# Kernel optimization log

Measured on AMD Instinct MI355X. Metric: run time of the kernel, lower is better.

Reference implementation:

```python
import jax, jax.numpy as jnp
import numpy as np

# Dims
B, C, D, H, W = 2, 64, 16, 64, 64
G = 2            # deformable groups (choose_group(64, 2) -> 2)
K = 27           # 3x3x3 kernel points
GC = C // G      # channels per group
AXIS = (0.5, 1.0, 1.0)   # offset_axis_scale (d, h, w)
EPS = 1e-5
# kernel point offsets for k=3, pad=1, dilation=1: {-1,0,1}^3
_KOFF = np.array([(a, b, c) for a in (-1, 0, 1) for b in (-1, 0, 1) for c in (-1, 0, 1)], dtype=np.float32)


def conv3d(x, w, b=None, pad=0):
    y = jax.lax.conv_general_dilated(x, w, (1, 1, 1), [(pad, pad)] * 3,
                                     dimension_numbers=('NCDHW', 'OIDHW', 'NCDHW'))
    if b is not None:
        y = y + b[None, :, None, None, None]
    return y


def proj1x1(x, w, b=None):
    y = jnp.einsum('oc,bcdhw->bodhw', w, x)
    if b is not None:
        y = y + b[None, :, None, None, None]
    return y


def _trilinear_sample(vflat, pd, ph, pw):
    # vflat: [B,G,GC,DHW]; pd/ph/pw: [B,G,DHW] float sampling coords; zeros padding outside
    d0 = jnp.floor(pd); h0 = jnp.floor(ph); w0 = jnp.floor(pw)
    td, th, tw = pd - d0, ph - h0, pw - w0
    d0 = d0.astype(jnp.int32); h0 = h0.astype(jnp.int32); w0 = w0.astype(jnp.int32)
    acc = jnp.zeros_like(vflat)
    for dd in (0, 1):
        for hh in (0, 1):
            for ww in (0, 1):
                di, hi, wi = d0 + dd, h0 + hh, w0 + ww
                valid = ((di >= 0) & (di < D) & (hi >= 0) & (hi < H) & (wi >= 0) & (wi < W)).astype(vflat.dtype)
                idx = (jnp.clip(di, 0, D - 1) * H + jnp.clip(hi, 0, H - 1)) * W + jnp.clip(wi, 0, W - 1)
                g = jnp.take_along_axis(vflat, jnp.broadcast_to(idx[:, :, None, :], vflat.shape), axis=3)
                wgt = ((td if dd else 1.0 - td) * (th if hh else 1.0 - th) * (tw if ww else 1.0 - tw)) * valid
                acc = acc + g * wgt[:, :, None, :]
    return acc


def setup_inputs() -> dict:
    key = jax.random.key(0)
    ks = jax.random.split(key, 8)
    f = jnp.float32
    s = 1.0 / np.sqrt(C)
    return {
        'x': jax.random.normal(ks[0], (B, C, D, H, W), f),
        'gate': jnp.zeros((), f),
        'pre_w': jax.random.normal(ks[1], (C, C, 1, 1, 1), f) * s,
        'post_w': jax.random.normal(ks[2], (C, C, 1, 1, 1), f) * s,
        'in_proj_w': jax.random.normal(ks[3], (C, C), f) * s,
        'in_proj_b': jnp.zeros((C,), f),
        'out_proj_w': jax.random.normal(ks[4], (C, C), f) * s,
        'out_proj_b': jnp.zeros((C,), f),
        'off_w': jax.random.normal(ks[5], (3 * G * K, C, 3, 3, 3), f) * 0.01,
        'off_b': jnp.zeros((3 * G * K,), f),
        'mask_w': jax.random.normal(ks[6], (G * K, C, 3, 3, 3), f) * 0.01,
        'mask_b': jnp.zeros((G * K,), f),
        'in_gamma': jnp.ones((C,), f),
        'in_beta': jnp.zeros((C,), f),
    }


def reference(x, gate, pre_w, post_w, in_proj_w, in_proj_b, out_proj_w, out_proj_b,
              off_w, off_b, mask_w, mask_b, in_gamma, in_beta):
    DHW = D * H * W
    xp = conv3d(x, pre_w)                                      # pre 1x1
    # --- DCNv3_3D: value projection, learned offsets + softmax modulation mask ---
    v = proj1x1(xp, in_proj_w, in_proj_b).reshape(B, G, GC, DHW)
    off = conv3d(xp, off_w, off_b, pad=1).reshape(B, G, K, 3, DHW)   # warmed-up offset_scale = 1.0
    m = jax.nn.softmax(conv3d(xp, mask_w, mask_b, pad=1).reshape(B, G, K, DHW), axis=2)
    dg, hg, wg = jnp.meshgrid(jnp.arange(D, dtype=jnp.float32),
                              jnp.arange(H, dtype=jnp.float32),
                              jnp.arange(W, dtype=jnp.float32), indexing='ij')
    dg, hg, wg = dg.reshape(-1), hg.reshape(-1), wg.reshape(-1)      # [DHW]
    out = jnp.zeros_like(v)
    for k in range(K):   # fixed small loop over 27 kernel points
        pd = dg + _KOFF[k, 0] + off[:, :, k, 0] * AXIS[0]
        ph = hg + _KOFF[k, 1] + off[:, :, k, 1] * AXIS[1]
        pw = wg + _KOFF[k, 2] + off[:, :, k, 2] * AXIS[2]
        out = out + _trilinear_sample(v, pd, ph, pw) * m[:, :, k, :][:, :, None, :]
    y = out.reshape(B, C, D, H, W)
    y = proj1x1(y, out_proj_w, out_proj_b)
    # InstanceNorm3d + GELU
    mu = y.mean(axis=(2, 3, 4), keepdims=True)
    var = y.var(axis=(2, 3, 4), keepdims=True)
    y = (y - mu) * jax.lax.rsqrt(var + EPS)
    y = y * in_gamma[None, :, None, None, None] + in_beta[None, :, None, None, None]
    y = jax.nn.gelu(y)
    y = conv3d(y, post_w)                                      # post 1x1
    return x + jax.nn.sigmoid(gate) * y
```

## Files before the change

kernel.cpp:

```cpp
#include <hip/hip_runtime.h>
#include <hip/hip_bf16.h>

typedef short short8 __attribute__((ext_vector_type(8)));
typedef float f32x4 __attribute__((ext_vector_type(4)));
typedef _Float16 h2 __attribute__((ext_vector_type(2)));
typedef __fp16 fp16x2 __attribute__((ext_vector_type(2)));

#if __has_builtin(__builtin_elementwise_fma)
#define FMA2H(a, b, c) __builtin_elementwise_fma((a), (b), (c))
#else
#define FMA2H(a, b, c) ((a) * (b) + (c))
#endif

namespace {
constexpr int Bn = 2, Cn = 64, Dn = 16, Hn = 64, Wn = 64;
constexpr int Gn = 2, Kn = 27, GCn = 32;
constexpr int DHW = Dn * Hn * Wn;
constexpr int OCn = 216;
constexpr int PD = 18, PH = 66, PW = 66;
constexpr float EPS = 1e-5f;

constexpr int SROWS = 4 * 66;
constexpr int SLICE_B = SROWS * 128;

constexpr size_t XPADH_OFF = 0;
constexpr size_t XPADH_B   = (size_t)Bn * PD * PH * PW * Cn * 2;
constexpr size_t WFRAG_OFF = XPADH_OFF + XPADH_B;
constexpr size_t WFRAG_B   = (size_t)54 * 16 * 64 * 16;
constexpr size_t WV_OFF    = WFRAG_OFF + WFRAG_B;
constexpr size_t WV_B      = 64 * 64 * 4;
constexpr size_t CONV_OFF  = WV_OFF + WV_B;
constexpr size_t CONV_B    = (size_t)Bn * OCn * DHW * 2;
constexpr size_t V_OFF     = CONV_OFF + CONV_B;
constexpr size_t V_B       = (size_t)Bn * Gn * DHW * GCn * 2;
constexpr size_t SAMP_OFF  = V_OFF + V_B;
constexpr size_t SAMP_B    = (size_t)Bn * Gn * DHW * GCn * 2;
constexpr size_t STAT_OFF  = SAMP_OFF + SAMP_B;
constexpr size_t VBH_OFF   = STAT_OFF + 4096;
constexpr size_t VFRAG_OFF = VBH_OFF + 256;
constexpr size_t OFRAG_OFF = VFRAG_OFF + 8192;
constexpr size_t PFRAG_OFF = OFRAG_OFF + 8192;
}

__device__ inline float b2f(short s) {
  union { float f; unsigned u; } x; x.u = ((unsigned)(unsigned short)s) << 16; return x.f;
}
__device__ inline short f2b(float f) {
  __hip_bfloat16 h = __float2bfloat16(f);
  union { __hip_bfloat16 h; short s; } x; x.h = h; return x.s;
}
__device__ inline int iclamp(int v, int lo, int hi) { return v < lo ? lo : (v > hi ? hi : v); }
__device__ inline h2 u2h2(unsigned u) {
  union { unsigned u; h2 h; } x; x.u = u; return x.h;
}
__device__ inline unsigned h2u(h2 h) {
  union { unsigned u; h2 h; } x; x.h = h; return x.u;
}
__device__ inline h2 pkrtz(float a, float b) {
#if __has_builtin(__builtin_amdgcn_cvt_pkrtz)
  union { fp16x2 p; h2 h; } x;
  x.p = __builtin_amdgcn_cvt_pkrtz(a, b);
  return x.h;
#else
  return (h2){(_Float16)a, (_Float16)b};
#endif
}

__global__ __launch_bounds__(256) void zerofill(uint4* __restrict__ p, int n16) {
  int i = blockIdx.x * 256 + threadIdx.x;
  if (i < n16) p[i] = make_uint4(0, 0, 0, 0);
}

__global__ __launch_bounds__(256) void fillpad(const float* __restrict__ x,
                                               __hip_bfloat16* __restrict__ xpadh) {
  int tid = threadIdx.x;
  int w5 = tid & 31, cq = tid >> 5;
  int p = blockIdx.x * 32 + w5;
  int b = blockIdx.y;
  int w = p & 63, h = (p >> 6) & 63, d = p >> 12;
  const float* xb = x + ((size_t)b * 64 + cq * 8) * DHW + p;
  short8 o8;
#pragma unroll
  for (int j = 0; j < 8; ++j) o8[j] = f2b(xb[(size_t)j * DHW]);
  __hip_bfloat16* ob = xpadh + (size_t)b * (PD * PH * PW * 64)
      + ((((size_t)(d + 1) * 66) + (h + 1)) * 66 + (w + 1)) * 64 + cq * 8;
  *(short8*)ob = o8;
}

__global__ __launch_bounds__(256) void fold_weights(
    const float* __restrict__ pre_w, const float* __restrict__ in_proj_w,
    const float* __restrict__ off_w, const float* __restrict__ mask_w,
    short8* __restrict__ Wfrag, float* __restrict__ Wv) {
  int i = blockIdx.x * 256 + threadIdx.x;
  if (i < 64 * 64) {
    int o = i >> 6, c = i & 63;
    float s = 0.f;
    for (int cp = 0; cp < 64; ++cp) s += in_proj_w[o * 64 + cp] * pre_w[cp * 64 + c];
    Wv[i] = s;
    return;
  }
  int t = i - 64 * 64;
  if (t >= 54 * 16 * 64) return;
  int l = t & 63; int rest = t >> 6;
  int mt = rest & 15; int ks = rest >> 4;
  int oc = mt * 16 + (l & 15);
  int tap = ks >> 1;
  int c0 = (ks & 1) * 32 + (l >> 4) * 8;
  float vals[8] = {0.f, 0.f, 0.f, 0.f, 0.f, 0.f, 0.f, 0.f};
  if (oc < OCn) {
    const float* cw = (oc < 162) ? (off_w + (size_t)oc * 64 * 27)
                                 : (mask_w + (size_t)(oc - 162) * 64 * 27);
#pragma unroll 1
    for (int cp = 0; cp < 64; ++cp) {
      float wv = cw[cp * 27 + tap];
      const float* pr = pre_w + cp * 64 + c0;
#pragma unroll
      for (int j = 0; j < 8; ++j) vals[j] += wv * pr[j];
    }
  }
  short8 o8;
#pragma unroll
  for (int j = 0; j < 8; ++j) o8[j] = f2b(vals[j]);
  Wfrag[t] = o8;
}

__global__ __launch_bounds__(256) void packfrag(
    const float* __restrict__ Wv, const float* __restrict__ Wout,
    const float* __restrict__ Wpost, const float* __restrict__ vb,
    short8* __restrict__ vfrag, short8* __restrict__ ofrag,
    short8* __restrict__ pfrag, h2* __restrict__ vbh) {
  int i = blockIdx.x * 256 + threadIdx.x;
  if (i < 32) vbh[i] = pkrtz(vb[2 * i], vb[2 * i + 1]);
  int which = i >> 9;
  int t = i & 511;
  int l = t & 63, mt = (t >> 6) & 3, ks = t >> 8;
  int m = mt * 16 + (l & 15);
  int k0 = ks * 32 + (l >> 4) * 8;
  const float* W = (which == 0) ? Wv : (which == 1) ? Wout : Wpost;
  short8 o;
#pragma unroll
  for (int j = 0; j < 8; ++j) o[j] = f2b(W[m * 64 + k0 + j]);
  if (which == 0) vfrag[t] = o;
  else if (which == 1) ofrag[t] = o;
  else pfrag[t] = o;
}

#define GEMM_MFMA_BODY(FRAG)                                                  \
  int wid = tid >> 6, l = tid & 63, lm = l & 15, lk = l >> 4;                 \
  f32x4 acc[4][4];                                                            \
  _Pragma("unroll")                                                           \
  for (int mt = 0; mt < 4; ++mt)                                              \
    _Pragma("unroll")                                                         \
    for (int nt = 0; nt < 4; ++nt) acc[mt][nt] = (f32x4){0.f, 0.f, 0.f, 0.f}; \
  _Pragma("unroll")                                                           \
  for (int ks = 0; ks < 2; ++ks) {                                            \
    short8 af[4], bf[4];                                                      \
    _Pragma("unroll")                                                         \
    for (int mt = 0; mt < 4; ++mt) af[mt] = FRAG[(ks * 4 + mt) * 64 + l];     \
    _Pragma("unroll")                                                         \
    for (int nt = 0; nt < 4; ++nt) {                                          \
      int sr = wid * 64 + nt * 16 + lm;                                       \
      int us = ks * 4 + lk;                                                   \
      bf[nt] = *(const short8*)(stg + sr * 128 + ((us ^ (sr & 7)) << 4));     \
    }                                                                         \
    _Pragma("unroll")                                                         \
    for (int mt = 0; mt < 4; ++mt)                                            \
      _Pragma("unroll")                                                       \
      for (int nt = 0; nt < 4; ++nt)                                          \
        acc[mt][nt] = __builtin_amdgcn_mfma_f32_16x16x32_bf16(af[mt], bf[nt], acc[mt][nt], 0, 0, 0); \
  }

__global__ __launch_bounds__(256) void vproj_mfma(
    const char* __restrict__ xpadh, const short8* __restrict__ vfrag,
    const h2* __restrict__ vbh, _Float16* __restrict__ v) {
  __shared__ char stg[32768];
  __shared__ char bnc[256 * 144];
  int tid = threadIdx.x;
  int p0 = blockIdx.x * 256, b = blockIdx.y;
  const char* xb = xpadh + (size_t)b * (PD * PH * PW * 128);
#pragma unroll
  for (int it = 0; it < 8; ++it) {
    int idx = it * 256 + tid;
    int s = idx >> 3, slot = idx & 7;
    int p = p0 + s, w = p & 63, h = (p >> 6) & 63, d = p >> 12;
    const char* g = xb + ((((size_t)(d + 1)) * 66 + (h + 1)) * 66 + (w + 1)) * 128 + slot * 16;
    *(uint4*)(stg + s * 128 + ((slot ^ (s & 7)) << 4)) = *(const uint4*)g;
  }
  __syncthreads();
  GEMM_MFMA_BODY(vfrag)
#pragma unroll
  for (int mt = 0; mt < 4; ++mt)
#pragma unroll
    for (int nt = 0; nt < 4; ++nt)
#pragma unroll
      for (int r = 0; r < 4; ++r) {
        int pos = wid * 64 + nt * 16 + lm;
        int oc = mt * 16 + lk * 4 + r;
        *(_Float16*)(bnc + pos * 144 + oc * 2) = (_Float16)acc[mt][nt][r];
      }
  __syncthreads();
  {
    int p = p0 + tid;
    const unsigned* brow = (const unsigned*)(bnc + tid * 144);
    char* vb0 = (char*)v + ((size_t)(b * 2 + 0) * DHW + p) * 64;
    char* vb1 = (char*)v + ((size_t)(b * 2 + 1) * DHW + p) * 64;
#pragma unroll
    for (int s = 0; s < 8; ++s) {
      uint4 ov;
      unsigned* po = (unsigned*)&ov;
#pragma unroll
      for (int j = 0; j < 4; ++j) {
        h2 hv = u2h2(brow[s * 4 + j]) + vbh[s * 4 + j];
        po[j] = h2u(hv);
      }
      if (s < 4) *(uint4*)(vb0 + s * 16) = ov;
      else       *(uint4*)(vb1 + (s - 4) * 16) = ov;
    }
  }
}

__global__ __launch_bounds__(512, 4) void conv_mfma(
    const char* __restrict__ xpadh, const char* __restrict__ wfrag,
    const float* __restrict__ off_b, const float* __restrict__ mask_b,
    __hip_bfloat16* __restrict__ convout) {
  __shared__ char lds[SLICE_B];
  int tid = threadIdx.x;
  int h0 = blockIdx.x * 2, d = blockIdx.y, b = blockIdx.z;

  int wid = tid >> 6, l = tid & 63;
  int wm = wid & 3, wn = wid >> 2;
  int lm = l & 15, lk = l >> 4;
  const char* abase = wfrag + ((size_t)((wm * 4) * 64 + l)) * 16;
  const char* xb = xpadh + (size_t)b * (PD * PH * PW * 128);

  f32x4 acc[4][4];
#pragma unroll
  for (int mt = 0; mt < 4; ++mt)
#pragma unroll
    for (int nt = 0; nt < 4; ++nt) acc[mt][nt] = (f32x4){0.f, 0.f, 0.f, 0.f};

  short8 A0[4], B0[4];

#define LOADA(KS)                                                             \
  {                                                                           \
    const char* ap_ = abase + (KS) * 16384;                                   \
    _Pragma("unroll")                                                         \
    for (int mt = 0; mt < 4; ++mt) A0[mt] = *(const short8*)(ap_ + mt * 1024); \
  }
  LOADA(0)

#pragma unroll 1
  for (int dd = 0; dd < 3; ++dd) {
    __syncthreads();
#pragma unroll
    for (int it = 0; it < 5; ++it) {
      int idx = it * 512 + tid;
      if (idx < SROWS * 8) {
        int s = idx >> 3, slot = idx & 7;
        int hp = s / 66, wx = s - hp * 66;
        const char* g = xb + ((((size_t)(d + dd)) * 66 + (h0 + hp)) * 66 + wx) * 128 + slot * 16;
        *(uint4*)(lds + s * 128 + ((slot ^ (s & 7)) << 4)) = *(const uint4*)g;
      }
    }
    __syncthreads();

#pragma unroll 1
    for (int tl = 0; tl < 9; ++tl) {
      int dh = tl / 3, dw = tl - dh * 3;
      int srow = (wn + dh) * 66 + dw;
#pragma unroll
      for (int ch = 0; ch < 2; ++ch) {
        int ks = dd * 18 + tl * 2 + ch;
        int uslot = 4 * ch + lk;
#pragma unroll
        for (int nt = 0; nt < 4; ++nt) {
          int sr = srow + nt * 16 + lm;
          B0[nt] = *(const short8*)(lds + sr * 128 + ((uslot ^ (sr & 7)) << 4));
        }
        __builtin_amdgcn_s_setprio(1);
#pragma unroll
        for (int mt = 0; mt < 4; ++mt)
#pragma unroll
          for (int nt = 0; nt < 4; ++nt)
            acc[mt][nt] = __builtin_amdgcn_mfma_f32_16x16x32_bf16(A0[mt], B0[nt], acc[mt][nt], 0, 0, 0);
        __builtin_amdgcn_s_setprio(0);
        if (ks + 1 < 54) LOADA(ks + 1)
      }
    }
  }
#undef LOADA

  int pbase = d * 4096 + (h0 + wn) * 64;
#pragma unroll
  for (int mt = 0; mt < 4; ++mt) {
    int oc0 = wm * 64 + mt * 16 + lk * 4;
#pragma unroll
    for (int r = 0; r < 4; ++r) {
      int oc = oc0 + r;
      if (oc < OCn) {
        float bias = (oc < 162) ? off_b[oc] : mask_b[oc - 162];
        size_t orow = ((size_t)b * OCn + oc) * DHW + pbase;
#pragma unroll
        for (int nt = 0; nt < 4; ++nt)
          convout[orow + nt * 16 + lm] = __float2bfloat16(acc[mt][nt][r] + bias);
      }
    }
  }
}

__global__ __launch_bounds__(256) void dcn_sample(
    const __hip_bfloat16* __restrict__ convout, const _Float16* __restrict__ v,
    short* __restrict__ sampled) {
  __shared__ short offm[108 * 64];
  int tid = threadIdx.x;
  int id = blockIdx.x;
  int bg = (id & 7) >> 1;
  int p0 = (((id >> 3) << 1) + (id & 1)) * 64;
  int b = bg >> 1, g = bg & 1;

  const __hip_bfloat16* cb = convout + (size_t)b * OCn * DHW;
#pragma unroll 1
  for (int idx = tid; idx < 108 * 8; idx += 256) {
    int row = idx >> 3, col = idx & 7;
    int oc = (row < 81) ? (g * 81 + row) : (162 + g * Kn + (row - 81));
    *(uint4*)(offm + row * 64 + col * 8) = *(const uint4*)(cb + (size_t)oc * DHW + p0 + col * 8);
  }
  __syncthreads();

  int pl = tid >> 2, q = tid & 3;
  int p = p0 + pl;
  int w = p & 63, h = (p >> 6) & 63, d = p >> 12;

  float msum = 0.f;
  h2 acc[4];
#pragma unroll
  for (int j = 0; j < 4; ++j) acc[j] = (h2){(_Float16)0.f, (_Float16)0.f};
  const char* vg = (const char*)v + ((size_t)bg * DHW * GCn + q * 8) * 2;

#pragma unroll 1
  for (int k = 0; k < Kn; ++k) {
    float offd = b2f(offm[(3 * k + 0) * 64 + pl]);
    float offh = b2f(offm[(3 * k + 1) * 64 + pl]);
    float offw = b2f(offm[(3 * k + 2) * 64 + pl]);
    float pd = (float)(d + (k / 9) - 1) + offd * 0.5f;
    float ph = (float)(h + ((k / 3) % 3) - 1) + offh;
    float pw = (float)(w + (k % 3) - 1) + offw;
    float fd = floorf(pd), fh = floorf(ph), fw = floorf(pw);
    float td = pd - fd, th = ph - fh, tw = pw - fw;
    int d0 = (int)fd, h0 = (int)fh, w0 = (int)fw;
    float ek = __expf(b2f(offm[(81 + k) * 64 + pl]));
    msum += ek;

    float wd0 = ((unsigned)d0 < (unsigned)Dn) ? (1.f - td) * ek : 0.f;
    float wd1 = ((unsigned)(d0 + 1) < (unsigned)Dn) ? td * ek : 0.f;
    float wh0 = ((unsigned)h0 < (unsigned)Hn) ? (1.f - th) : 0.f;
    float wh1 = ((unsigned)(h0 + 1) < (unsigned)Hn) ? th : 0.f;
    float ww0 = ((unsigned)w0 < (unsigned)Wn) ? (1.f - tw) : 0.f;
    float ww1 = ((unsigned)(w0 + 1) < (unsigned)Wn) ? tw : 0.f;
    int dr0 = iclamp(d0, 0, Dn - 1) << 18, dr1 = iclamp(d0 + 1, 0, Dn - 1) << 18;
    int hr0 = iclamp(h0, 0, Hn - 1) << 12, hr1 = iclamp(h0 + 1, 0, Hn - 1) << 12;
    int wc0 = iclamp(w0, 0, Wn - 1) << 6,  wc1 = iclamp(w0 + 1, 0, Wn - 1) << 6;
    float wdh00 = wd0 * wh0, wdh01 = wd0 * wh1, wdh10 = wd1 * wh0, wdh11 = wd1 * wh1;

#define CORNER(BOFF, WT)                                                \
    {                                                                   \
      _Float16 wh_ = (_Float16)(WT);                                    \
      h2 w2_ = {wh_, wh_};                                              \
      uint4 u_ = *(const uint4*)(vg + (BOFF));                          \
      acc[0] = FMA2H(u2h2(u_.x), w2_, acc[0]);                          \
      acc[1] = FMA2H(u2h2(u_.y), w2_, acc[1]);                          \
      acc[2] = FMA2H(u2h2(u_.z), w2_, acc[2]);                          \
      acc[3] = FMA2H(u2h2(u_.w), w2_, acc[3]);                          \
    }
    CORNER(dr0 + hr0 + wc0, wdh00 * ww0)
    CORNER(dr0 + hr0 + wc1, wdh00 * ww1)
    CORNER(dr0 + hr1 + wc0, wdh01 * ww0)
    CORNER(dr0 + hr1 + wc1, wdh01 * ww1)
    CORNER(dr1 + hr0 + wc0, wdh10 * ww0)
    CORNER(dr1 + hr0 + wc1, wdh10 * ww1)
    CORNER(dr1 + hr1 + wc0, wdh11 * ww0)
    CORNER(dr1 + hr1 + wc1, wdh11 * ww1)
#undef CORNER
  }

  float rs = 1.f / msum;
  short8 o8;
#pragma unroll
  for (int j = 0; j < 4; ++j) {
    o8[2 * j]     = f2b((float)acc[j][0] * rs);
    o8[2 * j + 1] = f2b((float)acc[j][1] * rs);
  }
  *(short8*)((char*)sampled + ((size_t)bg * DHW + p) * 64 + q * 16) = o8;
}

__global__ __launch_bounds__(256) void outproj_mfma(
    const short* __restrict__ sampled, const short8* __restrict__ ofrag,
    const float* __restrict__ ob, __hip_bfloat16* __restrict__ t) {
  __shared__ char stg[32768];
  __shared__ char bnc[256 * 144];
  int tid = threadIdx.x;
  int p0 = blockIdx.x * 256, b = blockIdx.y;
#pragma unroll
  for (int it = 0; it < 8; ++it) {
    int idx = it * 256 + tid;
    int s = idx >> 3, slot = idx & 7;
    int g = slot >> 2;
    const char* src = (const char*)sampled + ((size_t)(b * 2 + g) * DHW + p0 + s) * 64 + (slot & 3) * 16;
    *(uint4*)(stg + s * 128 + ((slot ^ (s & 7)) << 4)) = *(const uint4*)src;
  }
  __syncthreads();
  GEMM_MFMA_BODY(ofrag)
#pragma unroll
  for (int mt = 0; mt < 4; ++mt)
#pragma unroll
    for (int r = 0; r < 4; ++r) {
      int oc = mt * 16 + lk * 4 + r;
      float bias = ob[oc];
#pragma unroll
      for (int nt = 0; nt < 4; ++nt) {
        int pos = wid * 64 + nt * 16 + lm;
        *(short*)(bnc + pos * 144 + oc * 2) = f2b(acc[mt][nt][r] + bias);
      }
    }
  __syncthreads();
  {
    int c = tid & 63, pq = tid >> 6;
    short* trow = (short*)t + ((size_t)b * 64 + c) * DHW + p0 + pq * 64;
#pragma unroll
    for (int s8 = 0; s8 < 8; ++s8) {
      short8 o8;
#pragma unroll
      for (int j = 0; j < 8; ++j)
        o8[j] = *(const short*)(bnc + (pq * 64 + s8 * 8 + j) * 144 + c * 2);
      *(short8*)(trow + s8 * 8) = o8;
    }
  }
}

__global__ __launch_bounds__(256) void stats_k(const __hip_bfloat16* __restrict__ t,
                                               float* __restrict__ stat) {
  int bc = blockIdx.x;
  const short8* tc = (const short8*)(t + (size_t)bc * DHW);
  float s = 0.f, ss = 0.f;
  for (int i = threadIdx.x; i < DHW / 8; i += 256) {
    short8 s8 = tc[i];
#pragma unroll
    for (int j = 0; j < 8; ++j) { float xv = b2f(s8[j]); s += xv; ss += xv * xv; }
  }
#pragma unroll
  for (int o = 32; o > 0; o >>= 1) { s += __shfl_down(s, o); ss += __shfl_down(ss, o); }
  __shared__ float ls[4], lss[4];
  int wid = threadIdx.x >> 6;
  if ((threadIdx.x & 63) == 0) { ls[wid] = s; lss[wid] = ss; }
  __syncthreads();
  if (threadIdx.x == 0) {
    float S = ls[0] + ls[1] + ls[2] + ls[3];
    float SS = lss[0] + lss[1] + lss[2] + lss[3];
    float mu = S / (float)DHW;
    float var = SS / (float)DHW - mu * mu;
    stat[bc * 2 + 0] = mu;
    stat[bc * 2 + 1] = rsqrtf(var + EPS);
  }
}

__global__ __launch_bounds__(256) void normgelu(
    const __hip_bfloat16* __restrict__ t, const float* __restrict__ stat,
    const float* __restrict__ gamma, const float* __restrict__ beta,
    short* __restrict__ nvh) {
  int p = blockIdx.x * 256 + threadIdx.x;
  int b = blockIdx.y;
  short o[64];
#pragma unroll
  for (int c = 0; c < Cn; ++c) {
    float mu = stat[(b * Cn + c) * 2 + 0];
    float rstd = stat[(b * Cn + c) * 2 + 1];
    float tv = b2f(((const short*)t)[((size_t)b * Cn + c) * DHW + p]);
    float yv = (tv - mu) * rstd * gamma[c] + beta[c];
    float u = 0.7978845608028654f * (yv + 0.044715f * yv * yv * yv);
    float e = __expf(2.f * u);
    float th = 1.f - 2.f / (e + 1.f);
    o[c] = f2b(0.5f * yv * (1.f + th));
  }
  short* dst = nvh + ((size_t)b * DHW + p) * 64;
#pragma unroll
  for (int s8 = 0; s8 < 8; ++s8) {
    short8 o8;
#pragma unroll
    for (int j = 0; j < 8; ++j) o8[j] = o[s8 * 8 + j];
    *(short8*)(dst + s8 * 8) = o8;
  }
}

__global__ __launch_bounds__(256) void post_mfma(
    const short* __restrict__ nvh, const short8* __restrict__ pfrag,
    const float* __restrict__ x, const float* __restrict__ gate,
    float* __restrict__ out) {
  __shared__ char stg[32768];
  __shared__ char bnc[256 * 144];
  int tid = threadIdx.x;
  int p0 = blockIdx.x * 256, b = blockIdx.y;
#pragma unroll
  for (int it = 0; it < 8; ++it) {
    int idx = it * 256 + tid;
    int s = idx >> 3, slot = idx & 7;
    const char* src = (const char*)nvh + ((size_t)b * DHW + p0 + s) * 128 + slot * 16;
    *(uint4*)(stg + s * 128 + ((slot ^ (s & 7)) << 4)) = *(const uint4*)src;
  }
  __syncthreads();
  GEMM_MFMA_BODY(pfrag)
#pragma unroll
  for (int mt = 0; mt < 4; ++mt)
#pragma unroll
    for (int nt = 0; nt < 4; ++nt)
#pragma unroll
      for (int r = 0; r < 4; ++r) {
        int pos = wid * 64 + nt * 16 + lm;
        int oc = mt * 16 + lk * 4 + r;
        *(short*)(bnc + pos * 144 + oc * 2) = f2b(acc[mt][nt][r]);
      }
  __syncthreads();
  {
    float sg = 1.f / (1.f + __expf(-gate[0]));
    int c = tid & 63, pq = tid >> 6;
    size_t base = ((size_t)b * 64 + c) * DHW + p0 + pq * 64;
    const float4* x4 = (const float4*)(x + base);
    float4* o4 = (float4*)(out + base);
#pragma unroll
    for (int qd = 0; qd < 16; ++qd) {
      float4 xv = x4[qd];
      float v0 = b2f(*(const short*)(bnc + (pq * 64 + qd * 4 + 0) * 144 + c * 2));
      float v1 = b2f(*(const short*)(bnc + (pq * 64 + qd * 4 + 1) * 144 + c * 2));
      float v2 = b2f(*(const short*)(bnc + (pq * 64 + qd * 4 + 2) * 144 + c * 2));
      float v3 = b2f(*(const short*)(bnc + (pq * 64 + qd * 4 + 3) * 144 + c * 2));
      o4[qd] = make_float4(xv.x + sg * v0, xv.y + sg * v1, xv.z + sg * v2, xv.w + sg * v3);
    }
  }
}

extern "C" void kernel_launch(void* const* d_in, const int* in_sizes, int n_in,
                              void* d_out, int out_size, void* d_ws, size_t ws_size,
                              hipStream_t stream) {
  const float* x          = (const float*)d_in[0];
  const float* gate       = (const float*)d_in[1];
  const float* pre_w      = (const float*)d_in[2];
  const float* post_w     = (const float*)d_in[3];
  const float* in_proj_w  = (const float*)d_in[4];
  const float* in_proj_b  = (const float*)d_in[5];
  const float* out_proj_w = (const float*)d_in[6];
  const float* out_proj_b = (const float*)d_in[7];
  const float* off_w      = (const float*)d_in[8];
  const float* off_b      = (const float*)d_in[9];
  const float* mask_w     = (const float*)d_in[10];
  const float* mask_b     = (const float*)d_in[11];
  const float* in_gamma   = (const float*)d_in[12];
  const float* in_beta    = (const float*)d_in[13];

  char* ws = (char*)d_ws;
  __hip_bfloat16* xpadh = (__hip_bfloat16*)(ws + XPADH_OFF);
  short8* Wfrag  = (short8*)(ws + WFRAG_OFF);
  float* Wv      = (float*)(ws + WV_OFF);
  __hip_bfloat16* convout = (__hip_bfloat16*)(ws + CONV_OFF);
  _Float16* v    = (_Float16*)(ws + V_OFF);
  short* sampled = (short*)(ws + SAMP_OFF);
  short* nvh     = (short*)(ws + SAMP_OFF);
  float* stat    = (float*)(ws + STAT_OFF);
  h2* vbh        = (h2*)(ws + VBH_OFF);
  short8* vfrag  = (short8*)(ws + VFRAG_OFF);
  short8* ofrag  = (short8*)(ws + OFRAG_OFF);
  short8* pfrag  = (short8*)(ws + PFRAG_OFF);
  __hip_bfloat16* t = (__hip_bfloat16*)(ws + XPADH_OFF);
  float* out = (float*)d_out;

  int zf16 = (int)(XPADH_B / 16);
  zerofill<<<(zf16 + 255) / 256, 256, 0, stream>>>((uint4*)xpadh, zf16);
  fillpad<<<dim3(DHW / 32, Bn), 256, 0, stream>>>(x, xpadh);
  int foldN = (64 * 64 + 54 * 16 * 64 + 255) / 256;
  fold_weights<<<foldN, 256, 0, stream>>>(pre_w, in_proj_w, off_w, mask_w, Wfrag, Wv);
  packfrag<<<6, 256, 0, stream>>>(Wv, out_proj_w, post_w, in_proj_b,
                                  vfrag, ofrag, pfrag, vbh);
  vproj_mfma<<<dim3(DHW / 256, Bn), 256, 0, stream>>>((const char*)xpadh, vfrag, vbh, v);
  conv_mfma<<<dim3(32, 16, 2), 512, 0, stream>>>((const char*)xpadh, (const char*)Wfrag,
                                                 off_b, mask_b, convout);
  dcn_sample<<<4096, 256, 0, stream>>>(convout, v, sampled);
  outproj_mfma<<<dim3(DHW / 256, Bn), 256, 0, stream>>>(sampled, ofrag, out_proj_b, t);
  stats_k<<<Bn * Cn, 256, 0, stream>>>(t, stat);
  normgelu<<<dim3(DHW / 256, Bn), 256, 0, stream>>>(t, stat, in_gamma, in_beta, nvh);
  post_mfma<<<dim3(DHW / 256, Bn), 256, 0, stream>>>(nvh, pfrag, x, gate, out);
}
```

Baseline: 328.1 us.

## Double-buffer conv LDS via global_load_lds and fuse norm stats into outproj

The conv kernel now double-buffers its input slice in LDS and fills it with direct global-to-LDS loads, so the next depth slice is fetched while the MFMAs for the current one run. This removes the load-then-sync stall at the start of each depth step. Separately, the per-channel sum and sum-of-squares for the instance norm are accumulated inside outproj via LDS and global atomics, which removes the stats_k kernel and its extra pass over t. The costs are double the LDS per conv block, which may lower occupancy, atomic contention on 256 stat entries, and float sums whose order is no longer deterministic.

```diff
diff --git a/kernel.cpp b/kernel.cpp
--- a/kernel.cpp
+++ b/kernel.cpp
@@ -11,6 +11,10 @@
 #else
 #define FMA2H(a, b, c) ((a) * (b) + (c))
 #endif
+
+typedef const unsigned int __attribute__((address_space(1))) u32_g;
+typedef unsigned int __attribute__((address_space(3))) u32_s;
+#define GLDS16(gp, lp) __builtin_amdgcn_global_load_lds((u32_g*)(gp), (u32_s*)(lp), 16, 0, 0)
 
 namespace {
 constexpr int Bn = 2, Cn = 64, Dn = 16, Hn = 64, Wn = 64;
@@ -128,9 +132,10 @@
     const float* __restrict__ Wv, const float* __restrict__ Wout,
     const float* __restrict__ Wpost, const float* __restrict__ vb,
     short8* __restrict__ vfrag, short8* __restrict__ ofrag,
-    short8* __restrict__ pfrag, h2* __restrict__ vbh) {
+    short8* __restrict__ pfrag, h2* __restrict__ vbh, float* __restrict__ stat) {
   int i = blockIdx.x * 256 + threadIdx.x;
   if (i < 32) vbh[i] = pkrtz(vb[2 * i], vb[2 * i + 1]);
+  if (i >= 256 && i < 512) stat[i - 256] = 0.f;
   int which = i >> 9;
   int t = i & 511;
   int l = t & 63, mt = (t >> 6) & 3, ks = t >> 8;
@@ -223,7 +228,7 @@
     const char* __restrict__ xpadh, const char* __restrict__ wfrag,
     const float* __restrict__ off_b, const float* __restrict__ mask_b,
     __hip_bfloat16* __restrict__ convout) {
-  __shared__ char lds[SLICE_B];
+  __shared__ char lds[2 * SLICE_B];
   int tid = threadIdx.x;
   int h0 = blockIdx.x * 2, d = blockIdx.y, b = blockIdx.z;
 
@@ -247,22 +252,31 @@
     _Pragma("unroll")                                                         \
     for (int mt = 0; mt < 4; ++mt) A0[mt] = *(const short8*)(ap_ + mt * 1024); \
   }
+#define STAGE(DD, BUF)                                                        \
+  {                                                                           \
+    char* db_ = lds + (BUF) * SLICE_B + (wid << 10);                          \
+    _Pragma("unroll")                                                         \
+    for (int it = 0; it < 5; ++it) {                                          \
+      int idx = it * 512 + tid;                                               \
+      if (idx < SROWS * 8) {                                                  \
+        int s_ = idx >> 3, slot_ = idx & 7;                                   \
+        int hp_ = s_ / 66, wx_ = s_ - hp_ * 66;                               \
+        int sslot_ = slot_ ^ (s_ & 7);                                        \
+        const char* g_ = xb + ((((size_t)(d + (DD))) * 66 + (h0 + hp_)) * 66 + wx_) * 128 + sslot_ * 16; \
+        GLDS16(g_, db_ + it * 8192);                                          \
+      }                                                                       \
+    }                                                                         \
+  }
+
+  STAGE(0, 0)
   LOADA(0)
+  __syncthreads();
 
 #pragma unroll 1
   for (int dd = 0; dd < 3; ++dd) {
-    __syncthreads();
-#pragma unroll
-    for (int it = 0; it < 5; ++it) {
-      int idx = it * 512 + tid;
-      if (idx < SROWS * 8) {
-        int s = idx >> 3, slot = idx & 7;
-        int hp = s / 66, wx = s - hp * 66;
-        const char* g = xb + ((((size_t)(d + dd)) * 66 + (h0 + hp)) * 66 + wx) * 128 + slot * 16;
-        *(uint4*)(lds + s * 128 + ((slot ^ (s & 7)) << 4)) = *(const uint4*)g;
-      }
-    }
-    __syncthreads();
+    int buf = dd & 1;
+    if (dd < 2) STAGE(dd + 1, buf ^ 1)
+    const char* slice = lds + buf * SLICE_B;
 
 #pragma unroll 1
     for (int tl = 0; tl < 9; ++tl) {
@@ -275,7 +289,7 @@
 #pragma unroll
         for (int nt = 0; nt < 4; ++nt) {
           int sr = srow + nt * 16 + lm;
-          B0[nt] = *(const short8*)(lds + sr * 128 + ((uslot ^ (sr & 7)) << 4));
+          B0[nt] = *(const short8*)(slice + sr * 128 + ((uslot ^ (sr & 7)) << 4));
         }
         __builtin_amdgcn_s_setprio(1);
 #pragma unroll
@@ -287,8 +301,10 @@
         if (ks + 1 < 54) LOADA(ks + 1)
       }
     }
+    __syncthreads();
   }
 #undef LOADA
+#undef STAGE
 
   int pbase = d * 4096 + (h0 + wn) * 64;
 #pragma unroll
@@ -395,11 +411,14 @@
 
 __global__ __launch_bounds__(256) void outproj_mfma(
     const short* __restrict__ sampled, const short8* __restrict__ ofrag,
-    const float* __restrict__ ob, __hip_bfloat16* __restrict__ t) {
+    const float* __restrict__ ob, __hip_bfloat16* __restrict__ t,
+    float* __restrict__ stat) {
   __shared__ char stg[32768];
   __shared__ char bnc[256 * 144];
+  __shared__ float red[128];
   int tid = threadIdx.x;
   int p0 = blockIdx.x * 256, b = blockIdx.y;
+  if (tid < 128) red[tid] = 0.f;
 #pragma unroll
   for (int it = 0; it < 8; ++it) {
     int idx = it * 256 + tid;
@@ -426,41 +445,24 @@
   {
     int c = tid & 63, pq = tid >> 6;
     short* trow = (short*)t + ((size_t)b * 64 + c) * DHW + p0 + pq * 64;
+    float s = 0.f, ss = 0.f;
 #pragma unroll
     for (int s8 = 0; s8 < 8; ++s8) {
       short8 o8;
 #pragma unroll
-      for (int j = 0; j < 8; ++j)
-        o8[j] = *(const short*)(bnc + (pq * 64 + s8 * 8 + j) * 144 + c * 2);
+      for (int j = 0; j < 8; ++j) {
+        short sv = *(const short*)(bnc + (pq * 64 + s8 * 8 + j) * 144 + c * 2);
+        o8[j] = sv;
+        float fv = b2f(sv);
+        s += fv; ss += fv * fv;
+      }
       *(short8*)(trow + s8 * 8) = o8;
     }
-  }
-}
-
-__global__ __launch_bounds__(256) void stats_k(const __hip_bfloat16* __restrict__ t,
-                                               float* __restrict__ stat) {
-  int bc = blockIdx.x;
-  const short8* tc = (const short8*)(t + (size_t)bc * DHW);
-  float s = 0.f, ss = 0.f;
-  for (int i = threadIdx.x; i < DHW / 8; i += 256) {
-    short8 s8 = tc[i];
-#pragma unroll
-    for (int j = 0; j < 8; ++j) { float xv = b2f(s8[j]); s += xv; ss += xv * xv; }
-  }
-#pragma unroll
-  for (int o = 32; o > 0; o >>= 1) { s += __shfl_down(s, o); ss += __shfl_down(ss, o); }
-  __shared__ float ls[4], lss[4];
-  int wid = threadIdx.x >> 6;
-  if ((threadIdx.x & 63) == 0) { ls[wid] = s; lss[wid] = ss; }
-  __syncthreads();
-  if (threadIdx.x == 0) {
-    float S = ls[0] + ls[1] + ls[2] + ls[3];
-    float SS = lss[0] + lss[1] + lss[2] + lss[3];
-    float mu = S / (float)DHW;
-    float var = SS / (float)DHW - mu * mu;
-    stat[bc * 2 + 0] = mu;
-    stat[bc * 2 + 1] = rsqrtf(var + EPS);
-  }
+    atomicAdd(&red[c], s);
+    atomicAdd(&red[64 + c], ss);
+  }
+  __syncthreads();
+  if (tid < 128) atomicAdd(&stat[b * 128 + tid], red[tid]);
 }
 
 __global__ __launch_bounds__(256) void normgelu(
@@ -472,8 +474,9 @@
   short o[64];
 #pragma unroll
   for (int c = 0; c < Cn; ++c) {
-    float mu = stat[(b * Cn + c) * 2 + 0];
-    float rstd = stat[(b * Cn + c) * 2 + 1];
+    float mu = stat[b * 128 + c] * (1.f / (float)DHW);
+    float var = stat[b * 128 + 64 + c] * (1.f / (float)DHW) - mu * mu;
+    float rstd = rsqrtf(var + EPS);
     float tv = b2f(((const short*)t)[((size_t)b * Cn + c) * DHW + p]);
     float yv = (tv - mu) * rstd * gamma[c] + beta[c];
     float u = 0.7978845608028654f * (yv + 0.044715f * yv * yv * yv);
@@ -577,13 +580,12 @@
   int foldN = (64 * 64 + 54 * 16 * 64 + 255) / 256;
   fold_weights<<<foldN, 256, 0, stream>>>(pre_w, in_proj_w, off_w, mask_w, Wfrag, Wv);
   packfrag<<<6, 256, 0, stream>>>(Wv, out_proj_w, post_w, in_proj_b,
-                                  vfrag, ofrag, pfrag, vbh);
+                                  vfrag, ofrag, pfrag, vbh, stat);
   vproj_mfma<<<dim3(DHW / 256, Bn), 256, 0, stream>>>((const char*)xpadh, vfrag, vbh, v);
   conv_mfma<<<dim3(32, 16, 2), 512, 0, stream>>>((const char*)xpadh, (const char*)Wfrag,
                                                  off_b, mask_b, convout);
   dcn_sample<<<4096, 256, 0, stream>>>(convout, v, sampled);
-  outproj_mfma<<<dim3(DHW / 256, Bn), 256, 0, stream>>>(sampled, ofrag, out_proj_b, t);
-  stats_k<<<Bn * Cn, 256, 0, stream>>>(t, stat);
+  outproj_mfma<<<dim3(DHW / 256, Bn), 256, 0, stream>>>(sampled, ofrag, out_proj_b, t, stat);
   normgelu<<<dim3(DHW / 256, Bn), 256, 0, stream>>>(t, stat, in_gamma, in_beta, nvh);
   post_mfma<<<dim3(DHW / 256, Bn), 256, 0, stream>>>(nvh, pfrag, x, gate, out);
 }
```

Result: no change. 326.1 us (median of 2 runs) (-0.6%).
